# Kernel tuning notes

Measured on AMD Instinct MI355X. Metric: run time of the kernel, lower is better.

## Reference

```python
import jax, jax.numpy as jnp
import numpy as np

UNITS = 1024
D_Q = 1024
D_V = 1024


def setup_inputs() -> dict:
    key = jax.random.key(0)
    ks = jax.random.split(key, 8)
    B, S = 32, 2048
    query = jax.random.normal(ks[0], (B, D_Q), dtype=jnp.float32)
    values = jax.random.normal(ks[1], (B, S, D_V), dtype=jnp.float32)
    # Keras Dense params (glorot-ish scale for weights, zero bias init kept random-free)
    W1 = jax.random.normal(ks[2], (D_V, UNITS), dtype=jnp.float32) / np.sqrt(D_V)
    b1 = jnp.zeros((UNITS,), dtype=jnp.float32)
    W2 = jax.random.normal(ks[3], (D_Q, UNITS), dtype=jnp.float32) / np.sqrt(D_Q)
    b2 = jnp.zeros((UNITS,), dtype=jnp.float32)
    V = jax.random.normal(ks[4], (UNITS, 1), dtype=jnp.float32) / np.sqrt(UNITS)
    bV = jnp.zeros((1,), dtype=jnp.float32)
    return {"query": query, "values": values, "W1": W1, "b1": b1,
            "W2": W2, "b2": b2, "V": V, "bV": bV}


def reference(query, values, W1, b1, W2, b2, V, bV):
    # query: [B, d_q], values: [B, S, d_v]
    proj_v = jnp.einsum('bsd,du->bsu', values, W1) + b1        # [B, S, U]
    proj_q = (query @ W2 + b2)[:, None, :]                      # [B, 1, U]
    score = jnp.tanh(proj_v + proj_q) @ V + bV                  # [B, S, 1]
    attention_weights = jax.nn.softmax(score, axis=1)           # [B, S, 1]
    context_vector = jnp.sum(attention_weights * values, axis=1)  # [B, d_v]
    return (context_vector, attention_weights)
```

## Files before the change

kernel.cpp:

```cpp
#include <hip/hip_runtime.h>
#include <math.h>

#define B_  32
#define S_  2048
#define DV  1024
#define U_  1024

typedef __attribute__((ext_vector_type(8))) short bf16x8;
typedef __attribute__((ext_vector_type(4))) float f32x4;

__device__ inline unsigned short f2bf(float f) {
    unsigned int x = __float_as_uint(f);
    return (unsigned short)((x + 0x7fffu + ((x >> 16) & 1u)) >> 16);
}

__device__ inline float tanh_fast(float x) {
    float ax = fabsf(x);
    float e  = __expf(ax + ax);
    float t  = 1.0f - __fdividef(2.0f, e + 1.0f);
    return copysignf(t, x);
}

__global__ void init_kernel(const float* __restrict__ b1, const float* __restrict__ b2,
                            float* __restrict__ t, float* __restrict__ ctx,
                            float* __restrict__ scores) {
    int i = blockIdx.x * 256 + threadIdx.x;
    scores[i] = 0.f;
    if (i < B_ * U_) {
        int u = i & (U_ - 1);
        t[i]   = b1[u] + b2[u];
        ctx[i] = 0.f;
    }
}

__global__ void projq_kernel(const float* __restrict__ q, const float* __restrict__ W2,
                             float* __restrict__ t) {
    int b  = blockIdx.x;
    int ks = blockIdx.y;
    int tid = threadIdx.x;
    __shared__ float qs[256];
    qs[tid] = q[b * DV + ks * 256 + tid];
    __syncthreads();
    float a0 = 0.f, a1 = 0.f, a2 = 0.f, a3 = 0.f;
    const float* w = W2 + (size_t)(ks * 256) * U_;
    for (int d = 0; d < 256; ++d) {
        float qd = qs[d];
        const float* wr = w + (size_t)d * U_ + tid;
        a0 += qd * wr[0];
        a1 += qd * wr[256];
        a2 += qd * wr[512];
        a3 += qd * wr[768];
    }
    atomicAdd(&t[b * U_ + tid      ], a0);
    atomicAdd(&t[b * U_ + tid + 256], a1);
    atomicAdd(&t[b * U_ + tid + 512], a2);
    atomicAdd(&t[b * U_ + tid + 768], a3);
}

__global__ void cvt_values(const float* __restrict__ v, unsigned short* __restrict__ o) {
    size_t i = ((size_t)blockIdx.x * 256 + threadIdx.x) * 8;
    float4 f0 = *(const float4*)(v + i);
    float4 f1 = *(const float4*)(v + i + 4);
    union { unsigned short s[8]; uint4 u; } p;
    p.s[0] = f2bf(f0.x); p.s[1] = f2bf(f0.y); p.s[2] = f2bf(f0.z); p.s[3] = f2bf(f0.w);
    p.s[4] = f2bf(f1.x); p.s[5] = f2bf(f1.y); p.s[6] = f2bf(f1.z); p.s[7] = f2bf(f1.w);
    *(uint4*)(o + i) = p.u;
}

__global__ void prep_w1t(const float* __restrict__ W1, unsigned short* __restrict__ W1T) {
    __shared__ float tile[64][65];
    int k0 = blockIdx.x * 64, u0 = blockIdx.y * 64;
    int t = threadIdx.x;
    int lr = t >> 4, lc = (t & 15) * 4;
#pragma unroll
    for (int i = 0; i < 4; ++i) {
        float4 f = *(const float4*)&W1[(size_t)(k0 + lr + i * 16) * U_ + u0 + lc];
        tile[lr + i * 16][lc + 0] = f.x; tile[lr + i * 16][lc + 1] = f.y;
        tile[lr + i * 16][lc + 2] = f.z; tile[lr + i * 16][lc + 3] = f.w;
    }
    __syncthreads();
    int ur = t >> 2, kq = (t & 3) * 16;
    union { unsigned short s[8]; uint4 u; } p0, p1;
#pragma unroll
    for (int e = 0; e < 8; ++e) p0.s[e] = f2bf(tile[kq + e][ur]);
#pragma unroll
    for (int e = 0; e < 8; ++e) p1.s[e] = f2bf(tile[kq + 8 + e][ur]);
    unsigned short* dst = W1T + (size_t)(u0 + ur) * 1024 + k0 + kq;
    *(uint4*)dst       = p0.u;
    *(uint4*)(dst + 8) = p1.u;
}

template<bool ABF16>
__launch_bounds__(256, 2)
__global__ void scores_mfma(const void* __restrict__ aPtr,
                            const unsigned short* __restrict__ W1T,
                            const float* __restrict__ t,
                            const float* __restrict__ V,
                            float* __restrict__ scores) {
    __shared__ unsigned short sA[128 * 40];
    __shared__ unsigned short sB[256 * 40];
    __shared__ float fscore[128];

    const int tid  = threadIdx.x;
    const int lane = tid & 63;
    const int wave = tid >> 6;
    const int wm = wave & 1, wn = wave >> 1;
    const int l15 = lane & 15, lq = lane >> 4;

    const int id    = blockIdx.x;
    const int utile = (id >> 3) & 3;
    const int stile = (id & 7) | ((id >> 5) << 3);
    const size_t row0 = (size_t)stile * 128;
    const int b       = (int)(row0 >> 11);
    const int s_local = (int)(row0 & 2047);
    const int u0      = utile * 256;

    if (tid < 128) fscore[tid] = 0.f;

    const int ar = tid >> 1, ak = (tid & 1) << 4;
    const int br = tid >> 1, bk = (tid & 1) << 4;

    const float* Af = (const float*)aPtr + (row0 + ar) * 1024 + ak;
    const unsigned short* Ab = (const unsigned short*)aPtr + (row0 + ar) * 1024 + ak;
    const unsigned short* Bp0 = W1T + (size_t)(u0 + br) * 1024 + bk;
    const unsigned short* Bp1 = Bp0 + 128 * 1024;

    f32x4 acc[4][8];
#pragma unroll
    for (int i = 0; i < 4; ++i)
#pragma unroll
        for (int j = 0; j < 8; ++j) acc[i][j] = (f32x4)0.f;

    uint4 sa0, sa1, sb0, sb1, sb2, sb3;
    float4 fa0, fa1, fa2, fa3;

    if (ABF16) {
        sa0 = *(const uint4*)(Ab);
        sa1 = *(const uint4*)(Ab + 8);
    } else {
        fa0 = *(const float4*)(Af);
        fa1 = *(const float4*)(Af + 4);
        fa2 = *(const float4*)(Af + 8);
        fa3 = *(const float4*)(Af + 12);
    }
    sb0 = *(const uint4*)(Bp0);
    sb1 = *(const uint4*)(Bp0 + 8);
    sb2 = *(const uint4*)(Bp1);
    sb3 = *(const uint4*)(Bp1 + 8);

    for (int k0 = 0; k0 < 1024; k0 += 32) {
        __syncthreads();
        if (ABF16) {
            *(uint4*)&sA[ar * 40 + ak]     = sa0;
            *(uint4*)&sA[ar * 40 + ak + 8] = sa1;
        } else {
            union { unsigned short s[8]; uint4 u; } p0, p1;
            p0.s[0] = f2bf(fa0.x); p0.s[1] = f2bf(fa0.y); p0.s[2] = f2bf(fa0.z); p0.s[3] = f2bf(fa0.w);
            p0.s[4] = f2bf(fa1.x); p0.s[5] = f2bf(fa1.y); p0.s[6] = f2bf(fa1.z); p0.s[7] = f2bf(fa1.w);
            p1.s[0] = f2bf(fa2.x); p1.s[1] = f2bf(fa2.y); p1.s[2] = f2bf(fa2.z); p1.s[3] = f2bf(fa2.w);
            p1.s[4] = f2bf(fa3.x); p1.s[5] = f2bf(fa3.y); p1.s[6] = f2bf(fa3.z); p1.s[7] = f2bf(fa3.w);
            *(uint4*)&sA[ar * 40 + ak]     = p0.u;
            *(uint4*)&sA[ar * 40 + ak + 8] = p1.u;
        }
        *(uint4*)&sB[br * 40 + bk]           = sb0;
        *(uint4*)&sB[br * 40 + bk + 8]       = sb1;
        *(uint4*)&sB[(br + 128) * 40 + bk]     = sb2;
        *(uint4*)&sB[(br + 128) * 40 + bk + 8] = sb3;

        if (k0 + 32 < 1024) {
            int nk = k0 + 32;
            if (ABF16) {
                sa0 = *(const uint4*)(Ab + nk);
                sa1 = *(const uint4*)(Ab + nk + 8);
            } else {
                fa0 = *(const float4*)(Af + nk);
                fa1 = *(const float4*)(Af + nk + 4);
                fa2 = *(const float4*)(Af + nk + 8);
                fa3 = *(const float4*)(Af + nk + 12);
            }
            sb0 = *(const uint4*)(Bp0 + nk);
            sb1 = *(const uint4*)(Bp0 + nk + 8);
            sb2 = *(const uint4*)(Bp1 + nk);
            sb3 = *(const uint4*)(Bp1 + nk + 8);
        }
        __syncthreads();

        bf16x8 af[4];
#pragma unroll
        for (int i = 0; i < 4; ++i)
            af[i] = *(const bf16x8*)&sA[(64 * wm + 16 * i + l15) * 40 + lq * 8];
#pragma unroll
        for (int j = 0; j < 8; ++j) {
            bf16x8 bfj = *(const bf16x8*)&sB[(128 * wn + 16 * j + l15) * 40 + lq * 8];
#pragma unroll
            for (int i = 0; i < 4; ++i)
                acc[i][j] = __builtin_amdgcn_mfma_f32_16x16x32_bf16(af[i], bfj, acc[i][j], 0, 0, 0);
        }
    }

    float tu[8], vu[8];
#pragma unroll
    for (int j = 0; j < 8; ++j) {
        int u = u0 + 128 * wn + 16 * j + l15;
        tu[j] = t[b * U_ + u];
        vu[j] = V[u];
    }
#pragma unroll
    for (int i = 0; i < 4; ++i) {
#pragma unroll
        for (int r = 0; r < 4; ++r) {
            float p = 0.f;
#pragma unroll
            for (int j = 0; j < 8; ++j) p += tanh_fast(acc[i][j][r] + tu[j]) * vu[j];
            p += __shfl_xor(p, 1);
            p += __shfl_xor(p, 2);
            p += __shfl_xor(p, 4);
            p += __shfl_xor(p, 8);
            if (l15 == 0) atomicAdd(&fscore[64 * wm + 16 * i + lq * 4 + r], p);
        }
    }
    __syncthreads();
    if (tid < 128) atomicAdd(&scores[(size_t)b * S_ + s_local + tid], fscore[tid]);
}

__launch_bounds__(256, 2)
__global__ void scores_vec(const float* __restrict__ values, const float* __restrict__ W1,
                           const float* __restrict__ t, const float* __restrict__ V,
                           float* __restrict__ scores) {
    __shared__ float vA[16][132];
    __shared__ float vB[16][68];
    __shared__ float fscore[128];
    const int b   = blockIdx.y;
    const int s0  = blockIdx.x * 128;
    const int tid = threadIdx.x;
    const int tx  = tid & 15, ty = tid >> 4;
    if (tid < 128) fscore[tid] = 0.f;
    const float* vbase = values + ((size_t)b * S_ + s0) * (size_t)DV;
    const int lm = tid >> 2, lkq = (tid & 3) * 4;
    const int lbk = tid >> 4, lbj = (tid & 15) * 4;
    for (int nt = 0; nt < U_ / 64; ++nt) {
        const int u0 = nt * 64;
        float acc[8][4];
#pragma unroll
        for (int i = 0; i < 8; ++i)
#pragma unroll
            for (int j = 0; j < 4; ++j) acc[i][j] = 0.f;
        for (int k0 = 0; k0 < DV; k0 += 16) {
            __syncthreads();
            const float4 v0 = *(const float4*)(vbase + (size_t)lm * DV + k0 + lkq);
            const float4 v1 = *(const float4*)(vbase + (size_t)(lm + 64) * DV + k0 + lkq);
            vA[lkq + 0][lm] = v0.x; vA[lkq + 1][lm] = v0.y;
            vA[lkq + 2][lm] = v0.z; vA[lkq + 3][lm] = v0.w;
            vA[lkq + 0][lm + 64] = v1.x; vA[lkq + 1][lm + 64] = v1.y;
            vA[lkq + 2][lm + 64] = v1.z; vA[lkq + 3][lm + 64] = v1.w;
            *(float4*)&vB[lbk][lbj] = *(const float4*)(W1 + (size_t)(k0 + lbk) * U_ + u0 + lbj);
            __syncthreads();
#pragma unroll
            for (int k = 0; k < 16; ++k) {
                float4 va0 = *(const float4*)&vA[k][ty * 8];
                float4 va1 = *(const float4*)&vA[k][ty * 8 + 4];
                float4 vb  = *(const float4*)&vB[k][tx * 4];
                float a_[8] = {va0.x, va0.y, va0.z, va0.w, va1.x, va1.y, va1.z, va1.w};
                float b_[4] = {vb.x, vb.y, vb.z, vb.w};
#pragma unroll
                for (int i = 0; i < 8; ++i)
#pragma unroll
                    for (int j = 0; j < 4; ++j) acc[i][j] += a_[i] * b_[j];
            }
        }
        float tq[4], vv[4];
#pragma unroll
        for (int j = 0; j < 4; ++j) {
            int u = u0 + tx * 4 + j;
            tq[j] = t[b * U_ + u];
            vv[j] = V[u];
        }
#pragma unroll
        for (int i = 0; i < 8; ++i) {
            float p = 0.f;
#pragma unroll
            for (int j = 0; j < 4; ++j) p += tanhf(acc[i][j] + tq[j]) * vv[j];
            p += __shfl_down(p, 8, 16);
            p += __shfl_down(p, 4, 16);
            p += __shfl_down(p, 2, 16);
            p += __shfl_down(p, 1, 16);
            if (tx == 0) fscore[ty * 8 + i] += p;
        }
    }
    __syncthreads();
    if (tid < 128) scores[(size_t)b * S_ + s0 + tid] = fscore[tid];
}

__global__ void softmax_kernel(const float* __restrict__ scores, float* __restrict__ wout) {
    int b = blockIdx.x;
    int tid = threadIdx.x;
    __shared__ float red[256];
    float v[8];
    float m = -1e30f;
#pragma unroll
    for (int i = 0; i < 8; ++i) {
        v[i] = scores[(size_t)b * S_ + tid + i * 256];
        m = fmaxf(m, v[i]);
    }
    red[tid] = m; __syncthreads();
    for (int off = 128; off > 0; off >>= 1) {
        if (tid < off) red[tid] = fmaxf(red[tid], red[tid + off]);
        __syncthreads();
    }
    m = red[0];
    __syncthreads();
    float s = 0.f;
#pragma unroll
    for (int i = 0; i < 8; ++i) { v[i] = __expf(v[i] - m); s += v[i]; }
    red[tid] = s; __syncthreads();
    for (int off = 128; off > 0; off >>= 1) {
        if (tid < off) red[tid] += red[tid + off];
        __syncthreads();
    }
    float inv = 1.f / red[0];
#pragma unroll
    for (int i = 0; i < 8; ++i) wout[(size_t)b * S_ + tid + i * 256] = v[i] * inv;
}

__global__ void context_kernel(const float* __restrict__ values, const float* __restrict__ w,
                               float* __restrict__ ctx) {
    int b  = blockIdx.x;
    int dc = blockIdx.y;
    int sc = blockIdx.z;
    int tid = threadIdx.x;
    int d = dc * 256 + tid;
    __shared__ float ws_[256];
    ws_[tid] = w[(size_t)b * S_ + sc * 256 + tid];
    __syncthreads();
    float acc = 0.f;
    const float* vp = values + ((size_t)b * S_ + sc * 256) * (size_t)DV + d;
#pragma unroll 4
    for (int s = 0; s < 256; ++s) acc += ws_[s] * vp[(size_t)s * DV];
    atomicAdd(&ctx[b * DV + d], acc);
}

extern "C" void kernel_launch(void* const* d_in, const int* in_sizes, int n_in,
                              void* d_out, int out_size, void* d_ws, size_t ws_size,
                              hipStream_t stream) {
    const float* query  = (const float*)d_in[0];
    const float* values = (const float*)d_in[1];
    const float* W1     = (const float*)d_in[2];
    const float* b1     = (const float*)d_in[3];
    const float* W2     = (const float*)d_in[4];
    const float* b2     = (const float*)d_in[5];
    const float* V      = (const float*)d_in[6];

    float* out  = (float*)d_out;
    float* ctx  = out;
    float* wout = out + B_ * DV;

    char* ws = (char*)d_ws;
    const size_t W1T_BYTES = (size_t)U_ * DV * 2;
    const size_t T_BYTES   = (size_t)B_ * U_ * 4;
    const size_t SC_BYTES  = (size_t)B_ * S_ * 4;
    const size_t ABF_BYTES = (size_t)B_ * S_ * DV * 2;

    if (ws_size >= W1T_BYTES + T_BYTES + SC_BYTES + ABF_BYTES) {
        unsigned short* W1T = (unsigned short*)ws;
        float* t      = (float*)(ws + W1T_BYTES);
        float* scores = t + B_ * U_;
        unsigned short* Abf = (unsigned short*)(scores + B_ * S_);

        init_kernel   <<<dim3(256),      256, 0, stream>>>(b1, b2, t, ctx, scores);
        projq_kernel  <<<dim3(32, 4),    256, 0, stream>>>(query, W2, t);
        cvt_values    <<<dim3(32768),    256, 0, stream>>>(values, Abf);
        prep_w1t      <<<dim3(16, 16),   256, 0, stream>>>(W1, W1T);
        scores_mfma<true><<<dim3(2048),  256, 0, stream>>>(Abf, W1T, t, V, scores);
        softmax_kernel<<<dim3(32),       256, 0, stream>>>(scores, wout);
        context_kernel<<<dim3(32, 4, 8), 256, 0, stream>>>(values, wout, ctx);
    } else if (ws_size >= W1T_BYTES + T_BYTES + SC_BYTES) {
        unsigned short* W1T = (unsigned short*)ws;
        float* t      = (float*)(ws + W1T_BYTES);
        float* scores = t + B_ * U_;

        init_kernel   <<<dim3(256),      256, 0, stream>>>(b1, b2, t, ctx, scores);
        projq_kernel  <<<dim3(32, 4),    256, 0, stream>>>(query, W2, t);
        prep_w1t      <<<dim3(16, 16),   256, 0, stream>>>(W1, W1T);
        scores_mfma<false><<<dim3(2048), 256, 0, stream>>>(values, W1T, t, V, scores);
        softmax_kernel<<<dim3(32),       256, 0, stream>>>(scores, wout);
        context_kernel<<<dim3(32, 4, 8), 256, 0, stream>>>(values, wout, ctx);
    } else {
        float* t      = (float*)ws;
        float* scores = t + B_ * U_;

        init_kernel   <<<dim3(256),      256, 0, stream>>>(b1, b2, t, ctx, scores);
        projq_kernel  <<<dim3(32, 4),    256, 0, stream>>>(query, W2, t);
        scores_vec    <<<dim3(16, 32),   256, 0, stream>>>(values, W1, t, V, scores);
        softmax_kernel<<<dim3(32),       256, 0, stream>>>(scores, wout);
        context_kernel<<<dim3(32, 4, 8), 256, 0, stream>>>(values, wout, ctx);
    }
}
```

Before: 637.1 us.

## Fuse preprocessing kernels, use direct-to-LDS swizzled loads, drop score atomics

```diff
diff --git a/kernel.cpp b/kernel.cpp
--- a/kernel.cpp
+++ b/kernel.cpp
@@ -9,28 +9,256 @@
 typedef __attribute__((ext_vector_type(8))) short bf16x8;
 typedef __attribute__((ext_vector_type(4))) float f32x4;
 
-__device__ inline unsigned short f2bf(float f) {
+__device__ __forceinline__ unsigned short f2bf(float f) {
     unsigned int x = __float_as_uint(f);
     return (unsigned short)((x + 0x7fffu + ((x >> 16) & 1u)) >> 16);
 }
 
-__device__ inline float tanh_fast(float x) {
+__device__ __forceinline__ float tanh_fast(float x) {
     float ax = fabsf(x);
     float e  = __expf(ax + ax);
     float t  = 1.0f - __fdividef(2.0f, e + 1.0f);
     return copysignf(t, x);
 }
 
+__device__ __forceinline__ void gld16(void* lds, const void* g) {
+    __builtin_amdgcn_global_load_lds((const __attribute__((address_space(1))) unsigned int*)g,
+                                     (__attribute__((address_space(3))) unsigned int*)lds,
+                                     16, 0, 0);
+}
+
+__launch_bounds__(256)
+__global__ void pre_kernel(const float* __restrict__ values, unsigned short* __restrict__ Abf,
+                           const float* __restrict__ W1, unsigned short* __restrict__ W1T,
+                           const float* __restrict__ q, const float* __restrict__ W2,
+                           const float* __restrict__ b1, const float* __restrict__ b2,
+                           float* __restrict__ t) {
+    __shared__ float shbuf[64 * 65];
+    const int blk = blockIdx.x;
+    const int tid = threadIdx.x;
+
+    if (blk >= 288) {
+        size_t i = ((size_t)(blk - 288) * 256 + tid) * 8;
+        float4 f0 = *(const float4*)(values + i);
+        float4 f1 = *(const float4*)(values + i + 4);
+        union { unsigned short s[8]; uint4 u; } p;
+        p.s[0] = f2bf(f0.x); p.s[1] = f2bf(f0.y); p.s[2] = f2bf(f0.z); p.s[3] = f2bf(f0.w);
+        p.s[4] = f2bf(f1.x); p.s[5] = f2bf(f1.y); p.s[6] = f2bf(f1.z); p.s[7] = f2bf(f1.w);
+        *(uint4*)(Abf + i) = p.u;
+    } else if (blk < 256) {
+        const int k0 = (blk & 15) * 64, u0 = (blk >> 4) * 64;
+        const int lr = tid >> 4, lc = (tid & 15) * 4;
+#pragma unroll
+        for (int i = 0; i < 4; ++i) {
+            float4 f = *(const float4*)&W1[(size_t)(k0 + lr + i * 16) * U_ + u0 + lc];
+            shbuf[(lr + i * 16) * 65 + lc + 0] = f.x;
+            shbuf[(lr + i * 16) * 65 + lc + 1] = f.y;
+            shbuf[(lr + i * 16) * 65 + lc + 2] = f.z;
+            shbuf[(lr + i * 16) * 65 + lc + 3] = f.w;
+        }
+        __syncthreads();
+        const int ur = tid >> 2, kq = (tid & 3) * 16;
+        union { unsigned short s[8]; uint4 u; } p0, p1;
+#pragma unroll
+        for (int e = 0; e < 8; ++e) p0.s[e] = f2bf(shbuf[(kq + e) * 65 + ur]);
+#pragma unroll
+        for (int e = 0; e < 8; ++e) p1.s[e] = f2bf(shbuf[(kq + 8 + e) * 65 + ur]);
+        unsigned short* dst = W1T + (size_t)(u0 + ur) * 1024 + k0 + kq;
+        *(uint4*)dst       = p0.u;
+        *(uint4*)(dst + 8) = p1.u;
+    } else {
+        const int b = blk - 256;
+#pragma unroll
+        for (int i = 0; i < 4; ++i) shbuf[tid + i * 256] = q[b * DV + tid + i * 256];
+        __syncthreads();
+        float a0 = 0.f, a1 = 0.f, a2 = 0.f, a3 = 0.f;
+#pragma unroll 8
+        for (int d = 0; d < 1024; ++d) {
+            float qd = shbuf[d];
+            const float* wr = W2 + (size_t)d * U_ + tid;
+            a0 += qd * wr[0];
+            a1 += qd * wr[256];
+            a2 += qd * wr[512];
+            a3 += qd * wr[768];
+        }
+        t[b * U_ + tid      ] = a0 + b1[tid      ] + b2[tid      ];
+        t[b * U_ + tid + 256] = a1 + b1[tid + 256] + b2[tid + 256];
+        t[b * U_ + tid + 512] = a2 + b1[tid + 512] + b2[tid + 512];
+        t[b * U_ + tid + 768] = a3 + b1[tid + 768] + b2[tid + 768];
+    }
+}
+
+__launch_bounds__(256, 2)
+__global__ void scores_mfma(const unsigned short* __restrict__ Abf,
+                            const unsigned short* __restrict__ W1T,
+                            const float* __restrict__ t,
+                            const float* __restrict__ V,
+                            float* __restrict__ scores4) {
+    __shared__ __align__(16) unsigned short sAB[(128 + 256) * 32];
+    __shared__ float fscore[128];
+
+    const int tid  = threadIdx.x;
+    const int lane = tid & 63;
+    const int wv   = tid >> 6;
+    const int wm = wv & 1, wn = wv >> 1;
+    const int l15 = lane & 15, lq = lane >> 4;
+
+    const int id    = blockIdx.x;
+    const int utile = (id >> 3) & 3;
+    const int stile = (id & 7) | ((id >> 5) << 3);
+    const int row0  = stile * 128;
+    const int b     = row0 >> 11;
+    const int u0    = utile * 256;
+
+    if (tid < 128) fscore[tid] = 0.f;
+
+    const int srow = lane >> 2;
+    const int sc   = lane & 3;
+    const int arow0 = wv * 32 + srow;
+    const int arow1 = arow0 + 16;
+    unsigned short* ldsA0 = &sAB[arow0 * 32 + sc * 8];
+    unsigned short* ldsA1 = &sAB[arow1 * 32 + sc * 8];
+    const unsigned short* gA0 = Abf + (size_t)(row0 + arow0) * 1024 + (sc ^ ((arow0 >> 1) & 3)) * 8;
+    const unsigned short* gA1 = Abf + (size_t)(row0 + arow1) * 1024 + (sc ^ ((arow1 >> 1) & 3)) * 8;
+    unsigned short* ldsB_[4];
+    const unsigned short* gB_[4];
+#pragma unroll
+    for (int i = 0; i < 4; ++i) {
+        int br = wv * 64 + 16 * i + srow;
+        ldsB_[i] = &sAB[(128 + br) * 32 + sc * 8];
+        gB_[i]   = W1T + (size_t)(u0 + br) * 1024 + (sc ^ ((br >> 1) & 3)) * 8;
+    }
+
+    int aoff[4], boff[8];
+#pragma unroll
+    for (int i = 0; i < 4; ++i) {
+        int r = 64 * wm + 16 * i + l15;
+        aoff[i] = r * 32 + (lq ^ ((r >> 1) & 3)) * 8;
+    }
+#pragma unroll
+    for (int j = 0; j < 8; ++j) {
+        int r = 128 * wn + 16 * j + l15;
+        boff[j] = (128 + r) * 32 + (lq ^ ((r >> 1) & 3)) * 8;
+    }
+
+    f32x4 acc[4][8];
+#pragma unroll
+    for (int i = 0; i < 4; ++i)
+#pragma unroll
+        for (int j = 0; j < 8; ++j) acc[i][j] = (f32x4)0.f;
+
+    for (int ks = 0; ks < 32; ++ks) {
+        __syncthreads();
+        gld16(ldsA0, gA0);
+        gld16(ldsA1, gA1);
+        gld16(ldsB_[0], gB_[0]);
+        gld16(ldsB_[1], gB_[1]);
+        gld16(ldsB_[2], gB_[2]);
+        gld16(ldsB_[3], gB_[3]);
+        gA0 += 32; gA1 += 32;
+        gB_[0] += 32; gB_[1] += 32; gB_[2] += 32; gB_[3] += 32;
+        __syncthreads();
+
+        bf16x8 af[4];
+#pragma unroll
+        for (int i = 0; i < 4; ++i) af[i] = *(const bf16x8*)&sAB[aoff[i]];
+#pragma unroll
+        for (int j = 0; j < 8; ++j) {
+            bf16x8 bfj = *(const bf16x8*)&sAB[boff[j]];
+#pragma unroll
+            for (int i = 0; i < 4; ++i)
+                acc[i][j] = __builtin_amdgcn_mfma_f32_16x16x32_bf16(af[i], bfj, acc[i][j], 0, 0, 0);
+        }
+    }
+
+    float tu[8], vu[8];
+#pragma unroll
+    for (int j = 0; j < 8; ++j) {
+        int u = u0 + 128 * wn + 16 * j + l15;
+        tu[j] = t[b * U_ + u];
+        vu[j] = V[u];
+    }
+#pragma unroll
+    for (int i = 0; i < 4; ++i) {
+#pragma unroll
+        for (int r = 0; r < 4; ++r) {
+            float p = 0.f;
+#pragma unroll
+            for (int j = 0; j < 8; ++j) p += tanh_fast(acc[i][j][r] + tu[j]) * vu[j];
+            p += __shfl_xor(p, 1);
+            p += __shfl_xor(p, 2);
+            p += __shfl_xor(p, 4);
+            p += __shfl_xor(p, 8);
+            if (l15 == 0) atomicAdd(&fscore[64 * wm + 16 * i + lq * 4 + r], p);
+        }
+    }
+    __syncthreads();
+    if (tid < 128) scores4[(size_t)utile * (B_ * S_) + row0 + tid] = fscore[tid];
+}
+
+__global__ void softmax4_kernel(const float* __restrict__ s4, float* __restrict__ wout,
+                                float* __restrict__ ctx) {
+    int b = blockIdx.x;
+    int tid = threadIdx.x;
+#pragma unroll
+    for (int i = 0; i < 4; ++i) ctx[b * DV + tid + i * 256] = 0.f;
+    __shared__ float red[256];
+    float v[8];
+    float m = -1e30f;
+#pragma unroll
+    for (int i = 0; i < 8; ++i) {
+        size_t idx = (size_t)b * S_ + tid + i * 256;
+        v[i] = s4[idx] + s4[idx + 65536] + s4[idx + 131072] + s4[idx + 196608];
+        m = fmaxf(m, v[i]);
+    }
+    red[tid] = m; __syncthreads();
+    for (int off = 128; off > 0; off >>= 1) {
+        if (tid < off) red[tid] = fmaxf(red[tid], red[tid + off]);
+        __syncthreads();
+    }
+    m = red[0];
+    __syncthreads();
+    float s = 0.f;
+#pragma unroll
+    for (int i = 0; i < 8; ++i) { v[i] = __expf(v[i] - m); s += v[i]; }
+    red[tid] = s; __syncthreads();
+    for (int off = 128; off > 0; off >>= 1) {
+        if (tid < off) red[tid] += red[tid + off];
+        __syncthreads();
+    }
+    float inv = 1.f / red[0];
+#pragma unroll
+    for (int i = 0; i < 8; ++i) wout[(size_t)b * S_ + tid + i * 256] = v[i] * inv;
+}
+
+__global__ void context4_kernel(const float* __restrict__ values, const float* __restrict__ w,
+                                float* __restrict__ ctx) {
+    int b  = blockIdx.x;
+    int sc = blockIdx.y;
+    int tid = threadIdx.x;
+    __shared__ float ws_[256];
+    ws_[tid] = w[(size_t)b * S_ + sc * 256 + tid];
+    __syncthreads();
+    float4 acc = {0.f, 0.f, 0.f, 0.f};
+    const float* vp = values + ((size_t)b * S_ + sc * 256) * (size_t)DV + tid * 4;
+#pragma unroll 4
+    for (int s = 0; s < 256; ++s) {
+        float4 vv = *(const float4*)(vp + (size_t)s * DV);
+        float wv = ws_[s];
+        acc.x += wv * vv.x; acc.y += wv * vv.y; acc.z += wv * vv.z; acc.w += wv * vv.w;
+    }
+    atomicAdd(&ctx[b * DV + tid * 4 + 0], acc.x);
+    atomicAdd(&ctx[b * DV + tid * 4 + 1], acc.y);
+    atomicAdd(&ctx[b * DV + tid * 4 + 2], acc.z);
+    atomicAdd(&ctx[b * DV + tid * 4 + 3], acc.w);
+}
+
 __global__ void init_kernel(const float* __restrict__ b1, const float* __restrict__ b2,
-                            float* __restrict__ t, float* __restrict__ ctx,
-                            float* __restrict__ scores) {
+                            float* __restrict__ t, float* __restrict__ ctx) {
     int i = blockIdx.x * 256 + threadIdx.x;
-    scores[i] = 0.f;
-    if (i < B_ * U_) {
-        int u = i & (U_ - 1);
-        t[i]   = b1[u] + b2[u];
-        ctx[i] = 0.f;
-    }
+    int u = i & (U_ - 1);
+    t[i]   = b1[u] + b2[u];
+    ctx[i] = 0.f;
 }
 
 __global__ void projq_kernel(const float* __restrict__ q, const float* __restrict__ W2,
@@ -55,172 +283,6 @@
     atomicAdd(&t[b * U_ + tid + 256], a1);
     atomicAdd(&t[b * U_ + tid + 512], a2);
     atomicAdd(&t[b * U_ + tid + 768], a3);
-}
-
-__global__ void cvt_values(const float* __restrict__ v, unsigned short* __restrict__ o) {
-    size_t i = ((size_t)blockIdx.x * 256 + threadIdx.x) * 8;
-    float4 f0 = *(const float4*)(v + i);
-    float4 f1 = *(const float4*)(v + i + 4);
-    union { unsigned short s[8]; uint4 u; } p;
-    p.s[0] = f2bf(f0.x); p.s[1] = f2bf(f0.y); p.s[2] = f2bf(f0.z); p.s[3] = f2bf(f0.w);
-    p.s[4] = f2bf(f1.x); p.s[5] = f2bf(f1.y); p.s[6] = f2bf(f1.z); p.s[7] = f2bf(f1.w);
-    *(uint4*)(o + i) = p.u;
-}
-
-__global__ void prep_w1t(const float* __restrict__ W1, unsigned short* __restrict__ W1T) {
-    __shared__ float tile[64][65];
-    int k0 = blockIdx.x * 64, u0 = blockIdx.y * 64;
-    int t = threadIdx.x;
-    int lr = t >> 4, lc = (t & 15) * 4;
-#pragma unroll
-    for (int i = 0; i < 4; ++i) {
-        float4 f = *(const float4*)&W1[(size_t)(k0 + lr + i * 16) * U_ + u0 + lc];
-        tile[lr + i * 16][lc + 0] = f.x; tile[lr + i * 16][lc + 1] = f.y;
-        tile[lr + i * 16][lc + 2] = f.z; tile[lr + i * 16][lc + 3] = f.w;
-    }
-    __syncthreads();
-    int ur = t >> 2, kq = (t & 3) * 16;
-    union { unsigned short s[8]; uint4 u; } p0, p1;
-#pragma unroll
-    for (int e = 0; e < 8; ++e) p0.s[e] = f2bf(tile[kq + e][ur]);
-#pragma unroll
-    for (int e = 0; e < 8; ++e) p1.s[e] = f2bf(tile[kq + 8 + e][ur]);
-    unsigned short* dst = W1T + (size_t)(u0 + ur) * 1024 + k0 + kq;
-    *(uint4*)dst       = p0.u;
-    *(uint4*)(dst + 8) = p1.u;
-}
-
-template<bool ABF16>
-__launch_bounds__(256, 2)
-__global__ void scores_mfma(const void* __restrict__ aPtr,
-                            const unsigned short* __restrict__ W1T,
-                            const float* __restrict__ t,
-                            const float* __restrict__ V,
-                            float* __restrict__ scores) {
-    __shared__ unsigned short sA[128 * 40];
-    __shared__ unsigned short sB[256 * 40];
-    __shared__ float fscore[128];
-
-    const int tid  = threadIdx.x;
-    const int lane = tid & 63;
-    const int wave = tid >> 6;
-    const int wm = wave & 1, wn = wave >> 1;
-    const int l15 = lane & 15, lq = lane >> 4;
-
-    const int id    = blockIdx.x;
-    const int utile = (id >> 3) & 3;
-    const int stile = (id & 7) | ((id >> 5) << 3);
-    const size_t row0 = (size_t)stile * 128;
-    const int b       = (int)(row0 >> 11);
-    const int s_local = (int)(row0 & 2047);
-    const int u0      = utile * 256;
-
-    if (tid < 128) fscore[tid] = 0.f;
-
-    const int ar = tid >> 1, ak = (tid & 1) << 4;
-    const int br = tid >> 1, bk = (tid & 1) << 4;
-
-    const float* Af = (const float*)aPtr + (row0 + ar) * 1024 + ak;
-    const unsigned short* Ab = (const unsigned short*)aPtr + (row0 + ar) * 1024 + ak;
-    const unsigned short* Bp0 = W1T + (size_t)(u0 + br) * 1024 + bk;
-    const unsigned short* Bp1 = Bp0 + 128 * 1024;
-
-    f32x4 acc[4][8];
-#pragma unroll
-    for (int i = 0; i < 4; ++i)
-#pragma unroll
-        for (int j = 0; j < 8; ++j) acc[i][j] = (f32x4)0.f;
-
-    uint4 sa0, sa1, sb0, sb1, sb2, sb3;
-    float4 fa0, fa1, fa2, fa3;
-
-    if (ABF16) {
-        sa0 = *(const uint4*)(Ab);
-        sa1 = *(const uint4*)(Ab + 8);
-    } else {
-        fa0 = *(const float4*)(Af);
-        fa1 = *(const float4*)(Af + 4);
-        fa2 = *(const float4*)(Af + 8);
-        fa3 = *(const float4*)(Af + 12);
-    }
-    sb0 = *(const uint4*)(Bp0);
-    sb1 = *(const uint4*)(Bp0 + 8);
-    sb2 = *(const uint4*)(Bp1);
-    sb3 = *(const uint4*)(Bp1 + 8);
-
-    for (int k0 = 0; k0 < 1024; k0 += 32) {
-        __syncthreads();
-        if (ABF16) {
-            *(uint4*)&sA[ar * 40 + ak]     = sa0;
-            *(uint4*)&sA[ar * 40 + ak + 8] = sa1;
-        } else {
-            union { unsigned short s[8]; uint4 u; } p0, p1;
-            p0.s[0] = f2bf(fa0.x); p0.s[1] = f2bf(fa0.y); p0.s[2] = f2bf(fa0.z); p0.s[3] = f2bf(fa0.w);
-            p0.s[4] = f2bf(fa1.x); p0.s[5] = f2bf(fa1.y); p0.s[6] = f2bf(fa1.z); p0.s[7] = f2bf(fa1.w);
-            p1.s[0] = f2bf(fa2.x); p1.s[1] = f2bf(fa2.y); p1.s[2] = f2bf(fa2.z); p1.s[3] = f2bf(fa2.w);
-            p1.s[4] = f2bf(fa3.x); p1.s[5] = f2bf(fa3.y); p1.s[6] = f2bf(fa3.z); p1.s[7] = f2bf(fa3.w);
-            *(uint4*)&sA[ar * 40 + ak]     = p0.u;
-            *(uint4*)&sA[ar * 40 + ak + 8] = p1.u;
-        }
-        *(uint4*)&sB[br * 40 + bk]           = sb0;
-        *(uint4*)&sB[br * 40 + bk + 8]       = sb1;
-        *(uint4*)&sB[(br + 128) * 40 + bk]     = sb2;
-        *(uint4*)&sB[(br + 128) * 40 + bk + 8] = sb3;
-
-        if (k0 + 32 < 1024) {
-            int nk = k0 + 32;
-            if (ABF16) {
-                sa0 = *(const uint4*)(Ab + nk);
-                sa1 = *(const uint4*)(Ab + nk + 8);
-            } else {
-                fa0 = *(const float4*)(Af + nk);
-                fa1 = *(const float4*)(Af + nk + 4);
-                fa2 = *(const float4*)(Af + nk + 8);
-                fa3 = *(const float4*)(Af + nk + 12);
-            }
-            sb0 = *(const uint4*)(Bp0 + nk);
-            sb1 = *(const uint4*)(Bp0 + nk + 8);
-            sb2 = *(const uint4*)(Bp1 + nk);
-            sb3 = *(const uint4*)(Bp1 + nk + 8);
-        }
-        __syncthreads();
-
-        bf16x8 af[4];
-#pragma unroll
-        for (int i = 0; i < 4; ++i)
-            af[i] = *(const bf16x8*)&sA[(64 * wm + 16 * i + l15) * 40 + lq * 8];
-#pragma unroll
-        for (int j = 0; j < 8; ++j) {
-            bf16x8 bfj = *(const bf16x8*)&sB[(128 * wn + 16 * j + l15) * 40 + lq * 8];
-#pragma unroll
-            for (int i = 0; i < 4; ++i)
-                acc[i][j] = __builtin_amdgcn_mfma_f32_16x16x32_bf16(af[i], bfj, acc[i][j], 0, 0, 0);
-        }
-    }
-
-    float tu[8], vu[8];
-#pragma unroll
-    for (int j = 0; j < 8; ++j) {
-        int u = u0 + 128 * wn + 16 * j + l15;
-        tu[j] = t[b * U_ + u];
-        vu[j] = V[u];
-    }
-#pragma unroll
-    for (int i = 0; i < 4; ++i) {
-#pragma unroll
-        for (int r = 0; r < 4; ++r) {
-            float p = 0.f;
-#pragma unroll
-            for (int j = 0; j < 8; ++j) p += tanh_fast(acc[i][j][r] + tu[j]) * vu[j];
-            p += __shfl_xor(p, 1);
-            p += __shfl_xor(p, 2);
-            p += __shfl_xor(p, 4);
-            p += __shfl_xor(p, 8);
-            if (l15 == 0) atomicAdd(&fscore[64 * wm + 16 * i + lq * 4 + r], p);
-        }
-    }
-    __syncthreads();
-    if (tid < 128) atomicAdd(&scores[(size_t)b * S_ + s_local + tid], fscore[tid]);
 }
 
 __launch_bounds__(256, 2)
@@ -322,23 +384,6 @@
     for (int i = 0; i < 8; ++i) wout[(size_t)b * S_ + tid + i * 256] = v[i] * inv;
 }
 
-__global__ void context_kernel(const float* __restrict__ values, const float* __restrict__ w,
-                               float* __restrict__ ctx) {
-    int b  = blockIdx.x;
-    int dc = blockIdx.y;
-    int sc = blockIdx.z;
-    int tid = threadIdx.x;
-    int d = dc * 256 + tid;
-    __shared__ float ws_[256];
-    ws_[tid] = w[(size_t)b * S_ + sc * 256 + tid];
-    __syncthreads();
-    float acc = 0.f;
-    const float* vp = values + ((size_t)b * S_ + sc * 256) * (size_t)DV + d;
-#pragma unroll 4
-    for (int s = 0; s < 256; ++s) acc += ws_[s] * vp[(size_t)s * DV];
-    atomicAdd(&ctx[b * DV + d], acc);
-}
-
 extern "C" void kernel_launch(void* const* d_in, const int* in_sizes, int n_in,
                               void* d_out, int out_size, void* d_ws, size_t ws_size,
                               hipStream_t stream) {
@@ -357,41 +402,27 @@
     char* ws = (char*)d_ws;
     const size_t W1T_BYTES = (size_t)U_ * DV * 2;
     const size_t T_BYTES   = (size_t)B_ * U_ * 4;
-    const size_t SC_BYTES  = (size_t)B_ * S_ * 4;
+    const size_t S4_BYTES  = (size_t)4 * B_ * S_ * 4;
     const size_t ABF_BYTES = (size_t)B_ * S_ * DV * 2;
 
-    if (ws_size >= W1T_BYTES + T_BYTES + SC_BYTES + ABF_BYTES) {
+    if (ws_size >= W1T_BYTES + T_BYTES + S4_BYTES + ABF_BYTES) {
         unsigned short* W1T = (unsigned short*)ws;
-        float* t      = (float*)(ws + W1T_BYTES);
-        float* scores = t + B_ * U_;
-        unsigned short* Abf = (unsigned short*)(scores + B_ * S_);
-
-        init_kernel   <<<dim3(256),      256, 0, stream>>>(b1, b2, t, ctx, scores);
-        projq_kernel  <<<dim3(32, 4),    256, 0, stream>>>(query, W2, t);
-        cvt_values    <<<dim3(32768),    256, 0, stream>>>(values, Abf);
-        prep_w1t      <<<dim3(16, 16),   256, 0, stream>>>(W1, W1T);
-        scores_mfma<true><<<dim3(2048),  256, 0, stream>>>(Abf, W1T, t, V, scores);
-        softmax_kernel<<<dim3(32),       256, 0, stream>>>(scores, wout);
-        context_kernel<<<dim3(32, 4, 8), 256, 0, stream>>>(values, wout, ctx);
-    } else if (ws_size >= W1T_BYTES + T_BYTES + SC_BYTES) {
-        unsigned short* W1T = (unsigned short*)ws;
-        float* t      = (float*)(ws + W1T_BYTES);
-        float* scores = t + B_ * U_;
-
-        init_kernel   <<<dim3(256),      256, 0, stream>>>(b1, b2, t, ctx, scores);
-        projq_kernel  <<<dim3(32, 4),    256, 0, stream>>>(query, W2, t);
-        prep_w1t      <<<dim3(16, 16),   256, 0, stream>>>(W1, W1T);
-        scores_mfma<false><<<dim3(2048), 256, 0, stream>>>(values, W1T, t, V, scores);
-        softmax_kernel<<<dim3(32),       256, 0, stream>>>(scores, wout);
-        context_kernel<<<dim3(32, 4, 8), 256, 0, stream>>>(values, wout, ctx);
+        float* t       = (float*)(ws + W1T_BYTES);
+        float* scores4 = (float*)(ws + W1T_BYTES + T_BYTES);
+        unsigned short* Abf = (unsigned short*)(ws + W1T_BYTES + T_BYTES + S4_BYTES);
+
+        pre_kernel     <<<dim3(33056),  256, 0, stream>>>(values, Abf, W1, W1T, query, W2, b1, b2, t);
+        scores_mfma    <<<dim3(2048),   256, 0, stream>>>(Abf, W1T, t, V, scores4);
+        softmax4_kernel<<<dim3(32),     256, 0, stream>>>(scores4, wout, ctx);
+        context4_kernel<<<dim3(32, 8),  256, 0, stream>>>(values, wout, ctx);
     } else {
         float* t      = (float*)ws;
         float* scores = t + B_ * U_;
 
-        init_kernel   <<<dim3(256),      256, 0, stream>>>(b1, b2, t, ctx, scores);
+        init_kernel   <<<dim3(128),      256, 0, stream>>>(b1, b2, t, ctx);
         projq_kernel  <<<dim3(32, 4),    256, 0, stream>>>(query, W2, t);
         scores_vec    <<<dim3(16, 32),   256, 0, stream>>>(values, W1, t, V, scores);
         softmax_kernel<<<dim3(32),       256, 0, stream>>>(scores, wout);
-        context_kernel<<<dim3(32, 4, 8), 256, 0, stream>>>(values, wout, ctx);
-    }
-}
+        context4_kernel<<<dim3(32, 8),   256, 0, stream>>>(values, wout, ctx);
+    }
+}
```

Result: slower. 664.8 us (+4.3%).
